# Kernel optimization log

Measured on AMD Instinct MI355X. Metric: run time of the kernel, lower is better.

## Reference

```python
import jax, jax.numpy as jnp
import numpy as np

B, S, D, H, DC, HC = 2, 2048, 1024, 16, 64, 16  # batch, seq, hidden, heads, coord_dim, head_coord_dim
HD = D // H  # head_dim


def setup_inputs() -> dict:
    key = jax.random.key(0)
    ks = jax.random.split(key, 12)
    s = lambda fan_in: 1.0 / np.sqrt(fan_in)
    return {
        "hidden_states": jax.random.normal(ks[0], (B, S, D), jnp.float32),
        "coordinates": jax.random.normal(ks[1], (B, S, DC), jnp.float32),
        # weights stored [in, out] (used as x @ W + b, equivalent to torch Linear)
        "Wv": jax.random.uniform(ks[2], (D, D), jnp.float32, -s(D), s(D)),
        "bv": jax.random.uniform(ks[3], (D,), jnp.float32, -s(D), s(D)),
        "Wc": jax.random.uniform(ks[4], (DC, H * HC), jnp.float32, -s(DC), s(DC)),
        "bc": jax.random.uniform(ks[5], (H * HC,), jnp.float32, -s(DC), s(DC)),
        "Wn": jax.random.uniform(ks[6], (DC, DC), jnp.float32, -s(DC), s(DC)),
        "bn": jax.random.uniform(ks[7], (DC,), jnp.float32, -s(DC), s(DC)),
        "Wo": jax.random.uniform(ks[8], (D, D), jnp.float32, -s(D), s(D)),
        "bo": jax.random.uniform(ks[9], (D,), jnp.float32, -s(D), s(D)),
        "gamma": jax.random.normal(ks[10], (1, H, 1, 1), jnp.float32),
    }


def reference(hidden_states, coordinates, Wv, bv, Wc, bc, Wn, bn, Wo, bo, gamma):
    b, s, _ = hidden_states.shape
    # value: [B,H,S,HD]
    value = (hidden_states @ Wv + bv).reshape(b, s, H, HD).transpose(0, 2, 1, 3)
    # coord heads: [B,H,S,HC]
    z = (coordinates @ Wc + bc).reshape(b, s, H, HC).transpose(0, 2, 1, 3)
    z_sq = jnp.sum(z * z, axis=-1, keepdims=True)  # [B,H,S,1]
    sq_dist = z_sq + jnp.swapaxes(z_sq, -1, -2) - 2.0 * jnp.einsum("bhsc,bhtc->bhst", z, z)
    sq_dist = jnp.maximum(sq_dist, 0.0)
    g = jax.nn.softplus(gamma)  # [1,H,1,1]
    attn = jax.nn.softmax(-g * sq_dist, axis=-1)  # [B,H,S,S]
    out = jnp.einsum("bhst,bhtd->bhsd", attn, value)
    out = out.transpose(0, 2, 1, 3).reshape(b, s, D)
    updated_hidden = out @ Wo + bo
    updated_coords = coordinates @ Wn + bn
    return (updated_hidden, updated_coords)
```

## Files before the change

kernel.cpp:

```cpp
#include <hip/hip_runtime.h>
#include <hip/hip_bf16.h>

typedef short bf16x8 __attribute__((ext_vector_type(8)));
typedef float f32x4 __attribute__((ext_vector_type(4)));
typedef float f32x16 __attribute__((ext_vector_type(16)));
typedef unsigned short u16;
typedef unsigned int u32;

__device__ __forceinline__ u16 f2b(float f) {
  __hip_bfloat16 h = __float2bfloat16(f);
  return *reinterpret_cast<u16*>(&h);
}

#define MFMA16(a, b, c) __builtin_amdgcn_mfma_f32_16x16x32_bf16((a), (b), (c), 0, 0, 0)
#define MFMA32(a, b, c) __builtin_amdgcn_mfma_f32_32x32x16_bf16((a), (b), (c), 0, 0, 0)


__global__ void k_cvt(const float* __restrict__ in, u16* __restrict__ out, int n) {
  int i = (blockIdx.x * 256 + threadIdx.x) * 4;
  if (i >= n) return;
  float4 v = *reinterpret_cast<const float4*>(in + i);
  ushort4 o;
  o.x = f2b(v.x); o.y = f2b(v.y); o.z = f2b(v.z); o.w = f2b(v.w);
  *reinterpret_cast<ushort4*>(out + i) = o;
}

__global__ void k_wT(const float* __restrict__ W, u16* __restrict__ WT) {
  __shared__ float t[64][65];
  int tid = threadIdx.x;
  int r0 = (blockIdx.x & 15) << 6;
  int c0 = (blockIdx.x >> 4) << 6;
#pragma unroll
  for (int rep = 0; rep < 4; ++rep) {
    int e = tid + rep * 256;
    int r = e >> 4, c4 = (e & 15) << 2;
    float4 v = *reinterpret_cast<const float4*>(W + (size_t)(r0 + r) * 1024 + c0 + c4);
    t[r][c4] = v.x; t[r][c4 + 1] = v.y; t[r][c4 + 2] = v.z; t[r][c4 + 3] = v.w;
  }
  __syncthreads();
#pragma unroll
  for (int rep = 0; rep < 4; ++rep) {
    int e = tid + rep * 256;
    int c = e >> 4, r4 = (e & 15) << 2;
    ushort4 o;
    o.x = f2b(t[r4][c]); o.y = f2b(t[r4 + 1][c]);
    o.z = f2b(t[r4 + 2][c]); o.w = f2b(t[r4 + 3][c]);
    *reinterpret_cast<ushort4*>(WT + (size_t)(c0 + c) * 1024 + r0 + r4) = o;
  }
}

__global__ void k_z(const float* __restrict__ C, const float* __restrict__ Wc,
                    const float* __restrict__ bc, u16* __restrict__ Z,
                    float* __restrict__ zsq) {
  int gid = blockIdx.x * 256 + threadIdx.x;
  int bs = gid >> 4, h = gid & 15;
  const float* crow = C + (size_t)bs * 64;
  float acc[16];
#pragma unroll
  for (int c = 0; c < 16; ++c) acc[c] = bc[h * 16 + c];
  for (int k = 0; k < 64; ++k) {
    float cv = crow[k];
    const float* wr = Wc + (size_t)k * 256 + h * 16;
#pragma unroll
    for (int c = 0; c < 16; ++c) acc[c] = fmaf(cv, wr[c], acc[c]);
  }
  float sq = 0.f;
  u16 tmp[16];
#pragma unroll
  for (int c = 0; c < 16; ++c) { sq += acc[c] * acc[c]; tmp[c] = f2b(acc[c]); }
  int b = bs >> 11, s = bs & 2047;
  int bh = (b << 4) + h;
  u16* zr = Z + (((size_t)bh << 11) + s) * 16;
  *reinterpret_cast<uint4*>(zr) = *reinterpret_cast<uint4*>(tmp);
  *reinterpret_cast<uint4*>(zr + 8) = *reinterpret_cast<uint4*>(tmp + 8);
  zsq[((size_t)bh << 11) + s] = sq;
}

template <int OUTM>
__global__ __launch_bounds__(256) void k_gemm(const u16* __restrict__ A,
                                              const u16* __restrict__ BT,
                                              const float* __restrict__ bias,
                                              void* __restrict__ Cout,
                                              int M, int N, int K) {
  __shared__ u16 As[128][40];
  __shared__ u16 Bs[64][40];
  int nbn = N >> 6;
  int bm = blockIdx.x / nbn, bn = blockIdx.x % nbn;
  int tid = threadIdx.x, lane = tid & 63, w = tid >> 6;
  int wm = w >> 1, wn = w & 1;
  int l15 = lane & 15, lg = lane >> 4;
  f32x4 zero = {0.f, 0.f, 0.f, 0.f};
  f32x4 acc[4][2];
#pragma unroll
  for (int mi = 0; mi < 4; ++mi)
#pragma unroll
    for (int ni = 0; ni < 2; ++ni) acc[mi][ni] = zero;

  int ar = tid >> 2, aq = (tid & 3) << 3;
  const u16* Abase = A + (size_t)(bm * 128) * K;
  const u16* Bbase = BT + (size_t)(bn * 64) * K;

  for (int kk = 0; kk < K; kk += 32) {
    __syncthreads();
    *reinterpret_cast<uint4*>(&As[ar][aq]) =
        *reinterpret_cast<const uint4*>(Abase + (size_t)ar * K + kk + aq);
    *reinterpret_cast<uint4*>(&As[ar + 64][aq]) =
        *reinterpret_cast<const uint4*>(Abase + (size_t)(ar + 64) * K + kk + aq);
    *reinterpret_cast<uint4*>(&Bs[ar][aq]) =
        *reinterpret_cast<const uint4*>(Bbase + (size_t)ar * K + kk + aq);
    __syncthreads();
    bf16x8 af[4], bfr[2];
#pragma unroll
    for (int mi = 0; mi < 4; ++mi)
      af[mi] = *reinterpret_cast<const bf16x8*>(&As[wm * 64 + mi * 16 + l15][lg * 8]);
#pragma unroll
    for (int ni = 0; ni < 2; ++ni)
      bfr[ni] = *reinterpret_cast<const bf16x8*>(&Bs[wn * 32 + ni * 16 + l15][lg * 8]);
#pragma unroll
    for (int mi = 0; mi < 4; ++mi)
#pragma unroll
      for (int ni = 0; ni < 2; ++ni)
        acc[mi][ni] = MFMA16(af[mi], bfr[ni], acc[mi][ni]);
  }
#pragma unroll
  for (int mi = 0; mi < 4; ++mi) {
#pragma unroll
    for (int ni = 0; ni < 2; ++ni) {
      int col = bn * 64 + wn * 32 + ni * 16 + l15;
      float bb = bias[col];
#pragma unroll
      for (int j = 0; j < 4; ++j) {
        int row = bm * 128 + wm * 64 + mi * 16 + lg * 4 + j;
        float v = acc[mi][ni][j] + bb;
        if (OUTM == 0) {
          reinterpret_cast<float*>(Cout)[(size_t)row * N + col] = v;
        } else {
          int b = row >> 11, s = row & 2047, h = col >> 6, hd = col & 63;
          reinterpret_cast<u16*>(Cout)[((((size_t)(b * 16 + h) << 11) | s) << 6) + hd] = f2b(v);
        }
      }
    }
  }
}

__global__ void k_vF(const u16* __restrict__ V, u16* __restrict__ VF) {
  __shared__ u16 t[64][72];
  int tid = threadIdx.x;
  int bh = blockIdx.x >> 5;
  int s0 = (blockIdx.x & 31) << 6;
#pragma unroll
  for (int rep = 0; rep < 2; ++rep) {
    int e = tid + rep * 256;
    int sl = e >> 3, seg = (e & 7) << 3;
    *reinterpret_cast<uint4*>(&t[sl][seg]) =
        *reinterpret_cast<const uint4*>(V + ((size_t)(bh * 2048 + s0 + sl) << 6) + seg);
  }
  __syncthreads();
  int tg0 = (blockIdx.x & 31) << 2;
#pragma unroll
  for (int rep = 0; rep < 2; ++rep) {
    int c = tid + rep * 256;
    int l = c & 63;
    int dh = (c >> 6) & 1;
    int tgl = c >> 7;
    int l31 = l & 31, hi = l >> 5;
    u16 tmp[8];
#pragma unroll
    for (int j = 0; j < 8; ++j) tmp[j] = t[tgl * 16 + hi * 8 + j][dh * 32 + l31];
    size_t off = ((((size_t)bh * 128 + tg0 + tgl) * 2 + dh) << 9) + (l << 3);
    *reinterpret_cast<uint4*>(VF + off) = *reinterpret_cast<uint4*>(tmp);
  }
}

__global__ __launch_bounds__(256, 4) void k_attn(const u16* __restrict__ Z,
                                                 const float* __restrict__ zsq,
                                                 const u16* __restrict__ VF,
                                                 const float* __restrict__ gamma,
                                                 u16* __restrict__ O) {
  __shared__ __align__(16) char smem[17920];
  float* psqf = reinterpret_cast<float*>(smem + 17408);

  int tid = threadIdx.x, lane = tid & 63, w = tid >> 6;
  int l31 = lane & 31, hi = lane >> 5;
  int hi4 = hi << 2, hi8 = hi << 3;
  int th = w >> 1, qh = w & 1, th32 = th << 5;
  int bh = blockIdx.x >> 5, qt = blockIdx.x & 31;
  int q0 = qt << 6;
  int h = bh & 15, bb = bh >> 4;
  float gm = gamma[h];
  float g = (gm > 15.f) ? gm : log1pf(__expf(gm));
  float g2 = g * 1.4426950408889634f;

  const u16* Zb = Z + ((size_t)bh << 11) * 16;
  const float* zsb = zsq + ((size_t)bh << 11);
  const u16* VFb = VF + ((size_t)bh << 17);

  int q = (qh << 5) + l31;
  char* Prow = smem + q * 144;
  u32 psw = ((u32)(q >> 3) & 3u) << 4;

  uint4 zqu = *reinterpret_cast<const uint4*>(Zb + (size_t)(q0 + q) * 16 + hi8);
  zqu.x += 0x00800080u; zqu.y += 0x00800080u;
  zqu.z += 0x00800080u; zqu.w += 0x00800080u;
  bf16x8 zq2 = *reinterpret_cast<bf16x8*>(&zqu);

  bf16x8 aug_b;
  {
    float xq = -zsb[q0 + q];
    u32 xqu = __float_as_uint(xq);
    float xqh = __uint_as_float(xqu & 0xFFFF0000u);
    float xql = xq - xqh;
    u32 w1q = __builtin_amdgcn_perm(__float_as_uint(xql), xqu, 0x07060302u);
    uint4 abu = {0x3F803F80u, w1q, 0u, 0u};
    if (hi) { abu.x = 0u; abu.y = 0u; }
    aug_b = *reinterpret_cast<bf16x8*>(&abu);
  }

  const u16* zap = Zb + (size_t)(th32 + l31) * 16 + hi8;
  const float* xtp = zsb + th32 + l31;
  const u16* vwp = VFb + ((size_t)(th * 2) << 10) + (lane << 3);

  f32x16 oacc0 = {}, oacc1 = {};
  f32x4 psacc = {};

  bf16x8 zA_c = *reinterpret_cast<const bf16x8*>(zap);
  float zs_c = xtp[0];
  bf16x8 vb00_c = *reinterpret_cast<const bf16x8*>(vwp);
  bf16x8 vb10_c = *reinterpret_cast<const bf16x8*>(vwp + 512);

#pragma unroll 2
  for (int tt = 0; tt < 32; ++tt) {
    const int t0 = tt << 6;
    const u16* vtb = vwp + (tt << 12);
    bf16x8 vb01 = *reinterpret_cast<const bf16x8*>(vtb + 1024);
    bf16x8 vb11 = *reinterpret_cast<const bf16x8*>(vtb + 1024 + 512);
    bf16x8 zA_n = zA_c, vb00_n = vb00_c, vb10_n = vb10_c;
    float zs_n = zs_c;
    if (tt < 31) {
      zA_n = *reinterpret_cast<const bf16x8*>(zap + (size_t)(t0 + 64) * 16);
      zs_n = xtp[t0 + 64];
      vb00_n = *reinterpret_cast<const bf16x8*>(vtb + 4096);
      vb10_n = *reinterpret_cast<const bf16x8*>(vtb + 4096 + 512);
    }

    float xt = -zs_c;
    u32 xtu = __float_as_uint(xt);
    float xth = __uint_as_float(xtu & 0xFFFF0000u);
    float xtl = xt - xth;
    u32 w0 = __builtin_amdgcn_perm(__float_as_uint(xtl), xtu, 0x07060302u);
    uint4 aau = {w0, 0x3F803F80u, 0u, 0u};
    if (hi) { aau.x = 0u; aau.y = 0u; }
    bf16x8 aug_a = *reinterpret_cast<bf16x8*>(&aau);

    f32x16 sc = MFMA32(aug_a, aug_b, (f32x16){});
    sc = MFMA32(zA_c, zq2, sc);

#pragma unroll
    for (int g4 = 0; g4 < 4; ++g4) {
      float e0 = fminf(g2 * sc[g4 * 4 + 0], 0.f);
      float e1 = fminf(g2 * sc[g4 * 4 + 1], 0.f);
      float e2 = fminf(g2 * sc[g4 * 4 + 2], 0.f);
      float e3 = fminf(g2 * sc[g4 * 4 + 3], 0.f);
      float p0 = __builtin_amdgcn_exp2f(e0);
      float p1 = __builtin_amdgcn_exp2f(e1);
      float p2 = __builtin_amdgcn_exp2f(e2);
      float p3 = __builtin_amdgcn_exp2f(e3);
      psacc[0] += p0; psacc[1] += p1; psacc[2] += p2; psacc[3] += p3;
      u32 pk0, pk1;
      asm("v_cvt_pk_bf16_f32 %0, %1, %2" : "=v"(pk0) : "v"(p0), "v"(p1));
      asm("v_cvt_pk_bf16_f32 %0, %1, %2" : "=v"(pk1) : "v"(p2), "v"(p3));
      uint2 pkv = {pk0, pk1};
      int tcol = th32 + (g4 << 3) + hi4;
      *reinterpret_cast<uint2*>(Prow + (((u32)(tcol << 1)) ^ psw)) = pkv;
    }

    bf16x8 pa0 = *reinterpret_cast<const bf16x8*>(Prow + (((u32)((th32 + hi8) << 1)) ^ psw));
    bf16x8 pa1 = *reinterpret_cast<const bf16x8*>(Prow + (((u32)((th32 + 16 + hi8) << 1)) ^ psw));

    oacc0 = MFMA32(pa0, vb00_c, oacc0);
    oacc1 = MFMA32(pa0, vb10_c, oacc1);
    oacc0 = MFMA32(pa1, vb01, oacc0);
    oacc1 = MFMA32(pa1, vb11, oacc1);

    zA_c = zA_n; zs_c = zs_n; vb00_c = vb00_n; vb10_c = vb10_n;
  }

  float psum = (psacc[0] + psacc[1]) + (psacc[2] + psacc[3]);

  psum += __shfl_xor(psum, 32, 64);
  __syncthreads();
  if (w >= 2) {
    char* dst = smem + (w - 2) * 8192 + lane * 16;
#pragma unroll
    for (int c = 0; c < 4; ++c) {
      f32x4 v = {oacc0[c * 4 + 0], oacc0[c * 4 + 1], oacc0[c * 4 + 2], oacc0[c * 4 + 3]};
      *reinterpret_cast<f32x4*>(dst + c * 1024) = v;
    }
#pragma unroll
    for (int c = 0; c < 4; ++c) {
      f32x4 v = {oacc1[c * 4 + 0], oacc1[c * 4 + 1], oacc1[c * 4 + 2], oacc1[c * 4 + 3]};
      *reinterpret_cast<f32x4*>(dst + (c + 4) * 1024) = v;
    }
  }
  if (lane < 32) psqf[w * 32 + l31] = psum;
  __syncthreads();
  if (w < 2) {
    const char* src = smem + w * 8192 + lane * 16;
#pragma unroll
    for (int c = 0; c < 4; ++c) {
      f32x4 v = *reinterpret_cast<const f32x4*>(src + c * 1024);
      oacc0[c * 4 + 0] += v[0]; oacc0[c * 4 + 1] += v[1];
      oacc0[c * 4 + 2] += v[2]; oacc0[c * 4 + 3] += v[3];
    }
#pragma unroll
    for (int c = 0; c < 4; ++c) {
      f32x4 v = *reinterpret_cast<const f32x4*>(src + (c + 4) * 1024);
      oacc1[c * 4 + 0] += v[0]; oacc1[c * 4 + 1] += v[1];
      oacc1[c * 4 + 2] += v[2]; oacc1[c * 4 + 3] += v[3];
    }
#pragma unroll
    for (int g4 = 0; g4 < 4; ++g4) {
      f32x4 a = *reinterpret_cast<const f32x4*>(&psqf[qh * 32 + (g4 << 3) + hi4]);
      f32x4 b2 = *reinterpret_cast<const f32x4*>(&psqf[(qh + 2) * 32 + (g4 << 3) + hi4]);
#pragma unroll
      for (int j = 0; j < 4; ++j) {
        float inv = __builtin_amdgcn_rcpf(a[j] + b2[j]);
        int qrow = (g4 << 3) + hi4 + j;
        int srow = q0 + (qh << 5) + qrow;
        u16* orow = O + ((size_t)(bb * 2048 + srow) << 10) + h * 64 + l31;
        orow[0] = f2b(oacc0[g4 * 4 + j] * inv);
        orow[32] = f2b(oacc1[g4 * 4 + j] * inv);
      }
    }
  }
}

__global__ void k_coords(const float* __restrict__ C, const float* __restrict__ Wn,
                         const float* __restrict__ bn, float* __restrict__ out) {
  int gid = blockIdx.x * 256 + threadIdx.x;
  int bs = gid >> 6, c = gid & 63;
  const float* crow = C + (size_t)bs * 64;
  float acc = bn[c];
#pragma unroll 8
  for (int k = 0; k < 64; ++k) acc = fmaf(crow[k], Wn[k * 64 + c], acc);
  out[gid] = acc;
}

extern "C" void kernel_launch(void* const* d_in, const int* in_sizes, int n_in,
                              void* d_out, int out_size, void* d_ws, size_t ws_size,
                              hipStream_t stream) {
  const float* hs     = (const float*)d_in[0];
  const float* coords = (const float*)d_in[1];
  const float* Wv     = (const float*)d_in[2];
  const float* bv     = (const float*)d_in[3];
  const float* Wc     = (const float*)d_in[4];
  const float* bc     = (const float*)d_in[5];
  const float* Wn     = (const float*)d_in[6];
  const float* bn     = (const float*)d_in[7];
  const float* Wo     = (const float*)d_in[8];
  const float* bo     = (const float*)d_in[9];
  const float* gamma  = (const float*)d_in[10];
  float* out_h = (float*)d_out;
  float* out_c = out_h + 4194304;

  char* ws = (char*)d_ws;
  u16*   HSb  = (u16*)(ws + 0);
  u16*   O    = (u16*)(ws + 0);
  u16*   WvT  = (u16*)(ws + 8388608);
  u16*   WoT  = (u16*)(ws + 10485760);
  u16*   Zw   = (u16*)(ws + 12582912);
  float* zsqw = (float*)(ws + 14680064);
  u16*   Vw   = (u16*)(ws + 14942208);
  u16*   VFw  = (u16*)(ws + 23330816);

  k_cvt<<<4096, 256, 0, stream>>>(hs, HSb, 4194304);
  k_wT<<<256, 256, 0, stream>>>(Wv, WvT);
  k_wT<<<256, 256, 0, stream>>>(Wo, WoT);
  k_z<<<256, 256, 0, stream>>>(coords, Wc, bc, Zw, zsqw);
  k_gemm<1><<<512, 256, 0, stream>>>(HSb, WvT, bv, Vw, 4096, 1024, 1024);
  k_vF<<<1024, 256, 0, stream>>>(Vw, VFw);
  k_attn<<<1024, 256, 0, stream>>>(Zw, zsqw, VFw, gamma, O);
  k_gemm<0><<<512, 256, 0, stream>>>(O, WoT, bo, out_h, 4096, 1024, 1024);
  k_coords<<<1024, 256, 0, stream>>>(coords, Wn, bn, out_c);
}
```

Measured before the change: 132.8 us.

## Use direct global-to-LDS loads with XOR swizzle in GEMM, double-buffer attention P tile

The projection GEMM now loads A and B tiles straight into LDS with global_load_lds, instead of going through registers. It uses a 64-wide K step and an XOR-swizzled LDS layout to avoid bank conflicts, with two MFMA sub-steps per tile. The attention kernel alternates the P scratch area between two buffers on odd and even iterations. This is meant to reduce write-after-read hazards between iterations, at the cost of more shared memory. The larger K tile doubles the LDS footprint for the GEMM, which may lower occupancy.

Measured after the change: 121.3 us. 1.09x faster.

```diff
diff --git a/kernel.cpp b/kernel.cpp
--- a/kernel.cpp
+++ b/kernel.cpp
@@ -82,45 +82,60 @@
                                               const float* __restrict__ bias,
                                               void* __restrict__ Cout,
                                               int M, int N, int K) {
-  __shared__ u16 As[128][40];
-  __shared__ u16 Bs[64][40];
+  __shared__ u16 As[128 * 64];
+  __shared__ u16 Bs[64 * 64];
   int nbn = N >> 6;
   int bm = blockIdx.x / nbn, bn = blockIdx.x % nbn;
   int tid = threadIdx.x, lane = tid & 63, w = tid >> 6;
   int wm = w >> 1, wn = w & 1;
   int l15 = lane & 15, lg = lane >> 4;
-  f32x4 zero = {0.f, 0.f, 0.f, 0.f};
+  int lr = lane >> 3;
+  int swc = (lane & 7) ^ lr;
+
   f32x4 acc[4][2];
 #pragma unroll
   for (int mi = 0; mi < 4; ++mi)
 #pragma unroll
-    for (int ni = 0; ni < 2; ++ni) acc[mi][ni] = zero;
-
-  int ar = tid >> 2, aq = (tid & 3) << 3;
-  const u16* Abase = A + (size_t)(bm * 128) * K;
-  const u16* Bbase = BT + (size_t)(bn * 64) * K;
-
-  for (int kk = 0; kk < K; kk += 32) {
+    for (int ni = 0; ni < 2; ++ni) acc[mi][ni] = (f32x4){0.f, 0.f, 0.f, 0.f};
+
+  const u16* Abase = A + (size_t)(bm * 128) * K + (size_t)(w * 8 + lr) * K + swc * 8;
+  const u16* Bbase = BT + (size_t)(bn * 64) * K + (size_t)(w * 8 + lr) * K + swc * 8;
+  int rsw = l15 & 7;
+
+  for (int kk0 = 0; kk0 < K; kk0 += 64) {
     __syncthreads();
-    *reinterpret_cast<uint4*>(&As[ar][aq]) =
-        *reinterpret_cast<const uint4*>(Abase + (size_t)ar * K + kk + aq);
-    *reinterpret_cast<uint4*>(&As[ar + 64][aq]) =
-        *reinterpret_cast<const uint4*>(Abase + (size_t)(ar + 64) * K + kk + aq);
-    *reinterpret_cast<uint4*>(&Bs[ar][aq]) =
-        *reinterpret_cast<const uint4*>(Bbase + (size_t)ar * K + kk + aq);
+#pragma unroll
+    for (int i = 0; i < 4; ++i)
+      __builtin_amdgcn_global_load_lds(
+          (const __attribute__((address_space(1))) u32*)(Abase + (size_t)(i * 32) * K + kk0),
+          (__attribute__((address_space(3))) u32*)&As[(i * 32 + w * 8) * 64], 16, 0, 0);
+#pragma unroll
+    for (int i = 0; i < 2; ++i)
+      __builtin_amdgcn_global_load_lds(
+          (const __attribute__((address_space(1))) u32*)(Bbase + (size_t)(i * 32) * K + kk0),
+          (__attribute__((address_space(3))) u32*)&Bs[(i * 32 + w * 8) * 64], 16, 0, 0);
     __syncthreads();
-    bf16x8 af[4], bfr[2];
-#pragma unroll
-    for (int mi = 0; mi < 4; ++mi)
-      af[mi] = *reinterpret_cast<const bf16x8*>(&As[wm * 64 + mi * 16 + l15][lg * 8]);
-#pragma unroll
-    for (int ni = 0; ni < 2; ++ni)
-      bfr[ni] = *reinterpret_cast<const bf16x8*>(&Bs[wn * 32 + ni * 16 + l15][lg * 8]);
-#pragma unroll
-    for (int mi = 0; mi < 4; ++mi)
-#pragma unroll
-      for (int ni = 0; ni < 2; ++ni)
-        acc[mi][ni] = MFMA16(af[mi], bfr[ni], acc[mi][ni]);
+#pragma unroll
+    for (int kk = 0; kk < 2; ++kk) {
+      bf16x8 af[4], bfr[2];
+#pragma unroll
+      for (int mi = 0; mi < 4; ++mi) {
+        int row = wm * 64 + mi * 16 + l15;
+        int ch = (kk * 4 + lg) ^ rsw;
+        af[mi] = *reinterpret_cast<const bf16x8*>(&As[row * 64 + ch * 8]);
+      }
+#pragma unroll
+      for (int ni = 0; ni < 2; ++ni) {
+        int row = wn * 32 + ni * 16 + l15;
+        int ch = (kk * 4 + lg) ^ rsw;
+        bfr[ni] = *reinterpret_cast<const bf16x8*>(&Bs[row * 64 + ch * 8]);
+      }
+#pragma unroll
+      for (int mi = 0; mi < 4; ++mi)
+#pragma unroll
+        for (int ni = 0; ni < 2; ++ni)
+          acc[mi][ni] = MFMA16(af[mi], bfr[ni], acc[mi][ni]);
+    }
   }
 #pragma unroll
   for (int mi = 0; mi < 4; ++mi) {
@@ -177,8 +192,8 @@
                                                  const u16* __restrict__ VF,
                                                  const float* __restrict__ gamma,
                                                  u16* __restrict__ O) {
-  __shared__ __align__(16) char smem[17920];
-  float* psqf = reinterpret_cast<float*>(smem + 17408);
+  __shared__ __align__(16) char smem[18944];
+  float* psqf = reinterpret_cast<float*>(smem + 18432);
 
   int tid = threadIdx.x, lane = tid & 63, w = tid >> 6;
   int l31 = lane & 31, hi = lane >> 5;
@@ -231,6 +246,7 @@
 #pragma unroll 2
   for (int tt = 0; tt < 32; ++tt) {
     const int t0 = tt << 6;
+    char* Pr = Prow + ((tt & 1) ? 9216 : 0);
     const u16* vtb = vwp + (tt << 12);
     bf16x8 vb01 = *reinterpret_cast<const bf16x8*>(vtb + 1024);
     bf16x8 vb11 = *reinterpret_cast<const bf16x8*>(vtb + 1024 + 512);
@@ -271,11 +287,11 @@
       asm("v_cvt_pk_bf16_f32 %0, %1, %2" : "=v"(pk1) : "v"(p2), "v"(p3));
       uint2 pkv = {pk0, pk1};
       int tcol = th32 + (g4 << 3) + hi4;
-      *reinterpret_cast<uint2*>(Prow + (((u32)(tcol << 1)) ^ psw)) = pkv;
-    }
-
-    bf16x8 pa0 = *reinterpret_cast<const bf16x8*>(Prow + (((u32)((th32 + hi8) << 1)) ^ psw));
-    bf16x8 pa1 = *reinterpret_cast<const bf16x8*>(Prow + (((u32)((th32 + 16 + hi8) << 1)) ^ psw));
+      *reinterpret_cast<uint2*>(Pr + (((u32)(tcol << 1)) ^ psw)) = pkv;
+    }
+
+    bf16x8 pa0 = *reinterpret_cast<const bf16x8*>(Pr + (((u32)((th32 + hi8) << 1)) ^ psw));
+    bf16x8 pa1 = *reinterpret_cast<const bf16x8*>(Pr + (((u32)((th32 + 16 + hi8) << 1)) ^ psw));
 
     oacc0 = MFMA32(pa0, vb00_c, oacc0);
     oacc1 = MFMA32(pa0, vb10_c, oacc1);
```
